# Optimization experiments

Hardware: AMD Instinct MI355X
Metric: run time of the kernel (lower is better)

Reference implementation:

```python
import jax, jax.numpy as jnp
import numpy as np

N, E, G = 40000, 400000, 64
IN, ED, HID, HEADS, OUT = 2, 18, 64, 4, 3

def _glorot(key, shape):
    fan_in = shape[0]
    return jax.random.normal(key, shape, dtype=jnp.float32) / np.float32(np.sqrt(fan_in))

def setup_inputs():
    key = jax.random.key(0)
    ks = jax.random.split(key, 32)
    d1 = HEADS * HID  # 256
    return {
        "x": jax.random.normal(ks[0], (N, IN), jnp.float32),
        "edge_index": jax.random.randint(ks[1], (2, E), 0, N),
        "edge_attr": jax.random.normal(ks[2], (E, ED), jnp.float32),
        "batch": jnp.sort(jax.random.randint(ks[3], (N,), 0, G)),
        # conv1: TransformerConv(2 -> 64, heads=4, concat=True, beta=True, edge_dim=18)
        "Wq1": _glorot(ks[4], (IN, d1)), "bq1": jnp.zeros((d1,), jnp.float32),
        "Wk1": _glorot(ks[5], (IN, d1)), "bk1": jnp.zeros((d1,), jnp.float32),
        "Wv1": _glorot(ks[6], (IN, d1)), "bv1": jnp.zeros((d1,), jnp.float32),
        "We1": _glorot(ks[7], (ED, d1)),
        "Wskip1": _glorot(ks[8], (IN, d1)), "bskip1": jnp.zeros((d1,), jnp.float32),
        "Wbeta1": _glorot(ks[9], (3 * d1, 1)),
        # conv2: TransformerConv(256 -> 64, heads=1, concat=False, beta=True, edge_dim=18)
        "Wq2": _glorot(ks[10], (d1, HID)), "bq2": jnp.zeros((HID,), jnp.float32),
        "Wk2": _glorot(ks[11], (d1, HID)), "bk2": jnp.zeros((HID,), jnp.float32),
        "Wv2": _glorot(ks[12], (d1, HID)), "bv2": jnp.zeros((HID,), jnp.float32),
        "We2": _glorot(ks[13], (ED, HID)),
        "Wskip2": _glorot(ks[14], (d1, HID)), "bskip2": jnp.zeros((HID,), jnp.float32),
        "Wbeta2": _glorot(ks[15], (3 * HID, 1)),
        "Wlin": _glorot(ks[16], (HID, OUT)), "blin": jnp.zeros((OUT,), jnp.float32),
    }

def _tconv(x, src, dst, edge_attr, Wq, bq, Wk, bk, Wv, bv, We, Wskip, bskip, Wbeta, H, C, concat):
    # PyG TransformerConv with edge_dim, beta=True, root_weight=True (eval: dropout off)
    n = x.shape[0]
    q = (x @ Wq + bq).reshape(n, H, C)
    k = (x @ Wk + bk).reshape(n, H, C)
    v = (x @ Wv + bv).reshape(n, H, C)
    e = (edge_attr @ We).reshape(-1, H, C)              # [E,H,C]
    kj = k[src] + e                                      # key_j + edge
    alpha = jnp.einsum('ehc,ehc->eh', q[dst], kj) * (1.0 / (C ** 0.5))  # [E,H]
    # segment softmax over destination nodes
    amax = jax.ops.segment_max(alpha, dst, num_segments=n)
    ex = jnp.exp(alpha - amax[dst])
    den = jax.ops.segment_sum(ex, dst, num_segments=n)
    w = ex / (den[dst] + 1e-16)
    msg = (v[src] + e) * w[:, :, None]                   # [E,H,C]
    out = jax.ops.segment_sum(msg, dst, num_segments=n)  # [N,H,C]
    out = out.reshape(n, H * C) if concat else out.mean(axis=1)
    # beta-gated skip connection
    xr = x @ Wskip + bskip
    beta = jax.nn.sigmoid(jnp.concatenate([out, xr, out - xr], axis=-1) @ Wbeta)
    return beta * xr + (1.0 - beta) * out

def reference(x, edge_index, edge_attr, batch, Wq1, bq1, Wk1, bk1, Wv1, bv1, We1, Wskip1, bskip1, Wbeta1, Wq2, bq2, Wk2, bk2, Wv2, bv2, We2, Wskip2, bskip2, Wbeta2, Wlin, blin):
    src, dst = edge_index[0], edge_index[1]
    h = jax.nn.relu(_tconv(x, src, dst, edge_attr, Wq1, bq1, Wk1, bk1, Wv1, bv1, We1, Wskip1, bskip1, Wbeta1, HEADS, HID, True))
    h = jax.nn.relu(_tconv(h, src, dst, edge_attr, Wq2, bq2, Wk2, bk2, Wv2, bv2, We2, Wskip2, bskip2, Wbeta2, 1, HID, False))
    # global mean pool per graph
    s = jax.ops.segment_sum(h, batch, num_segments=G)
    cnt = jax.ops.segment_sum(jnp.ones((h.shape[0], 1), h.dtype), batch, num_segments=G)
    pooled = s / jnp.maximum(cnt, 1.0)
    return pooled @ Wlin + blin
```

## Files before the change

### kernel.cpp

```cpp
#include <hip/hip_runtime.h>
#include <hip/hip_fp16.h>

#define N_NODES 40000
#define N_EDGES 400000
#define N_GRAPHS 64
#define D1 256
#define HIDC 64
#define NHEADS 4
#define EDIM 18
#define EPAD 20
#define OUTF 3

typedef _Float16 f16x8 __attribute__((ext_vector_type(8)));
typedef float f32x4 __attribute__((ext_vector_type(4)));

__global__ void prep_w(const float* __restrict__ Wq, const float* __restrict__ bq,
                       const float* __restrict__ Wk, const float* __restrict__ bk,
                       const float* __restrict__ Wv, const float* __restrict__ bv,
                       const float* __restrict__ Ws, const float* __restrict__ bs,
                       const float* __restrict__ We2,
                       const float* __restrict__ Wq1, const float* __restrict__ bq1,
                       const float* __restrict__ Wk1, const float* __restrict__ bk1,
                       const float* __restrict__ We1,
                       __half* __restrict__ Bt, float* __restrict__ bias,
                       float* __restrict__ cbuf) {
    int c = blockIdx.x, k = threadIdx.x;
    if (c < 256) {
        int m = c >> 6, d = c & 63;
        const float* W = (m == 0) ? Wq : (m == 1) ? Wk : (m == 2) ? Wv : Ws;
        Bt[c * 256 + k] = __float2half(W[k * 64 + d]);
        if (k == 0) {
            const float* b = (m == 0) ? bq : (m == 1) ? bk : (m == 2) ? bv : bs;
            bias[c] = b[d];
        }
    } else if (c < 288) {
        int j = c - 256;
        float s = 0.f;
        if (j < EDIM)
            for (int cc = 0; cc < 64; ++cc) s += Wq[k * 64 + cc] * We2[j * 64 + cc];
        Bt[c * 256 + k] = __float2half(s);
        if (k == 0) {
            float b = 0.f;
            if (j < EDIM)
                for (int cc = 0; cc < 64; ++cc) b += bq[cc] * We2[j * 64 + cc];
            bias[c] = b;
        }
    } else {
        int t = k;
        if (t < 36) {
            int h = t / 9, r = t % 9, a = r / 3, b = r % 3;
            const float* A = (a == 0) ? Wq1 : (a == 1) ? Wq1 + D1 : bq1;
            const float* B = (b == 0) ? Wk1 : (b == 1) ? Wk1 + D1 : bk1;
            float s = 0.f;
            for (int cc = 0; cc < 64; ++cc) s += A[h * 64 + cc] * B[h * 64 + cc];
            cbuf[h * 63 + a * 3 + b] = s;
        } else if (t < 252) {
            int i = t - 36;
            int h = i / 54, rr = (i % 54) / 18, j = i % 18;
            const float* A = (rr == 0) ? Wq1 : (rr == 1) ? Wq1 + D1 : bq1;
            float s = 0.f;
            for (int cc = 0; cc < 64; ++cc) s += A[h * 64 + cc] * We1[j * D1 + h * 64 + cc];
            cbuf[h * 63 + 9 + rr * 18 + j] = s;
        }
    }
}

__global__ void initA(const float* __restrict__ x, const float* __restrict__ cbuf,
                      float* __restrict__ coef, float* __restrict__ acc1,
                      float* __restrict__ acc2, float* __restrict__ out2,
                      int* __restrict__ deg, float* __restrict__ pooled,
                      int* __restrict__ gs, int* __restrict__ ge) {
    int t = blockIdx.x * 256 + threadIdx.x;
    acc1[t] = 0.f;
    {
        int n = t / 84, r = t % 84, h = r / 21, c = r % 21;
        const float* cb = cbuf + h * 63;
        float x0 = x[2 * n], x1 = x[2 * n + 1], o;
        if (c < 3) o = x0 * cb[c] + x1 * cb[3 + c] + cb[6 + c];
        else { int j = c - 3; o = x0 * cb[9 + j] + x1 * cb[27 + j] + cb[45 + j]; }
        coef[t] = o;
    }
    if (t < N_NODES * 64) out2[t] = 0.f;
    if (t < N_NODES * 20) acc2[t] = 0.f;
    if (t < N_NODES) deg[t] = 0;
    if (t < N_GRAPHS * HIDC) pooled[t] = 0.f;
    if (t < N_GRAPHS) { gs[t] = 0; ge[t] = 0; }
}

__global__ void hist_kernel(const int* __restrict__ ei, int* __restrict__ deg) {
    int e = blockIdx.x * 256 + threadIdx.x;
    if (e < N_EDGES) atomicAdd(&deg[ei[N_EDGES + e]], 1);
}

__global__ void scanA(const int* __restrict__ deg, int* __restrict__ bsum) {
    __shared__ int s[256];
    int b = blockIdx.x, t = threadIdx.x;
    s[t] = (t < 160) ? deg[b * 160 + t] : 0;
    __syncthreads();
    for (int off = 128; off; off >>= 1) {
        if (t < off) s[t] += s[t + off];
        __syncthreads();
    }
    if (t == 0) bsum[b] = s[0];
}

__global__ void scanB(const int* __restrict__ bsum, int* __restrict__ boff) {
    __shared__ int s[256];
    int t = threadIdx.x;
    int v = (t < 250) ? bsum[t] : 0;
    s[t] = v;
    __syncthreads();
    for (int off = 1; off < 256; off <<= 1) {
        int add = (t >= off) ? s[t - off] : 0;
        __syncthreads();
        s[t] += add;
        __syncthreads();
    }
    if (t < 250) boff[t] = s[t] - v;
}

__global__ void scanC(const int* __restrict__ deg, const int* __restrict__ boff,
                      int* __restrict__ cursor) {
    __shared__ int s[256];
    int b = blockIdx.x, t = threadIdx.x;
    int v = (t < 160) ? deg[b * 160 + t] : 0;
    s[t] = v;
    __syncthreads();
    for (int off = 1; off < 256; off <<= 1) {
        int add = (t >= off) ? s[t - off] : 0;
        __syncthreads();
        s[t] += add;
        __syncthreads();
    }
    if (t < 160) cursor[b * 160 + t] = boff[b] + s[t] - v;
}

__global__ void perm_kernel(const int* __restrict__ ei, int* __restrict__ cursor,
                            int* __restrict__ inv) {
    int e = blockIdx.x * 256 + threadIdx.x;
    if (e >= N_EDGES) return;
    int p = atomicAdd(&cursor[ei[N_EDGES + e]], 1);
    inv[p] = e;
}

__global__ void gatherE(const int* __restrict__ inv, const int* __restrict__ ei,
                        const float* __restrict__ ea, const float* __restrict__ x,
                        const float* __restrict__ coef,
                        int* __restrict__ src_s, int* __restrict__ dst_s,
                        float* __restrict__ ea_s, float* __restrict__ alpha1) {
    int p = blockIdx.x * 256 + threadIdx.x;
    if (p >= N_EDGES) return;
    int e = inv[p];
    int src = ei[e], dst = ei[N_EDGES + e];
    src_s[p] = src;
    dst_s[p] = dst;
    const float* srow = ea + (size_t)e * EDIM;
    float s[EDIM];
    #pragma unroll
    for (int j = 0; j < EDIM; ++j) s[j] = srow[j];
    float x0 = x[src * 2], x1 = x[src * 2 + 1];
    float4* drow = (float4*)(ea_s + (size_t)p * EPAD);
    drow[0] = make_float4(s[0],  s[1],  s[2],  s[3]);
    drow[1] = make_float4(s[4],  s[5],  s[6],  s[7]);
    drow[2] = make_float4(s[8],  s[9],  s[10], s[11]);
    drow[3] = make_float4(s[12], s[13], s[14], s[15]);
    drow[4] = make_float4(s[16], s[17], x0, x1);
    const float* cb = coef + (size_t)dst * 84;
    #pragma unroll
    for (int h = 0; h < NHEADS; ++h) {
        const float* c = cb + h * 21;
        float a = x0 * c[0] + x1 * c[1] + c[2];
        #pragma unroll
        for (int j = 0; j < EDIM; ++j) a += s[j] * c[3 + j];
        alpha1[(size_t)h * N_EDGES + p] = __expf(a * 0.125f);
    }
}

__global__ void strip1(const int* __restrict__ dst_s, const float* __restrict__ alpha1,
                       const float* __restrict__ ea_s, float* __restrict__ acc1) {
    int t = threadIdx.x;
    int strip = blockIdx.x * 2 + (t >> 7);
    int gl = t & 127;
    bool active = gl < 84;
    int cgl = active ? gl : 83;
    int h = cgl / 21, comp = cgl % 21;
    int voff = (comp == 0) ? 18 : (comp == 1) ? 19 : (comp - 3);
    bool isone = (comp == 2);
    int p0 = strip * 16;
    int dsts[16]; float w[16]; float v[16];
    #pragma unroll
    for (int j = 0; j < 16; ++j) dsts[j] = dst_s[p0 + j];
    #pragma unroll
    for (int j = 0; j < 16; ++j) w[j] = alpha1[(size_t)h * N_EDGES + p0 + j];
    #pragma unroll
    for (int j = 0; j < 16; ++j) v[j] = isone ? 1.f : ea_s[(size_t)(p0 + j) * EPAD + voff];
    float acc = 0.f;
    int prev = dsts[0];
    #pragma unroll
    for (int j = 0; j < 16; ++j) {
        if (dsts[j] != prev) {
            if (active) atomicAdd(&acc1[(size_t)prev * 84 + gl], acc);
            acc = 0.f; prev = dsts[j];
        }
        acc += w[j] * v[j];
    }
    if (active) atomicAdd(&acc1[(size_t)prev * 84 + gl], acc);
}

__global__ void finalize1x(const float* __restrict__ x, const float* __restrict__ acc1,
                           const float* __restrict__ Wv, const float* __restrict__ bv,
                           const float* __restrict__ We, const float* __restrict__ Wskip,
                           const float* __restrict__ bskip, const float* __restrict__ Wbeta,
                           __half* __restrict__ h1f) {
    __shared__ float red[4][4];
    int nb = blockIdx.x * 4;
    int t = threadIdx.x;
    int h = t >> 6;
    float wv0 = Wv[t], wv1 = Wv[D1 + t], bvv = bv[t];
    float we[EDIM];
    #pragma unroll
    for (int j = 0; j < EDIM; ++j) we[j] = We[j * D1 + t];
    float ws0 = Wskip[t], ws1 = Wskip[D1 + t], bsv = bskip[t];
    float wb0 = Wbeta[t], wb1 = Wbeta[D1 + t], wb2 = Wbeta[2 * D1 + t];
    float o[4], xr[4], part[4];
    #pragma unroll
    for (int i = 0; i < 4; ++i) {
        int node = nb + i;
        const float* a = acc1 + (size_t)node * 84 + h * 21;
        float l = a[2];
        float oo = a[0] * wv0 + a[1] * wv1 + l * bvv;
        #pragma unroll
        for (int j = 0; j < EDIM; ++j) oo += a[3 + j] * we[j];
        oo /= (l + 1e-16f);
        float x0 = x[node * 2], x1 = x[node * 2 + 1];
        xr[i] = x0 * ws0 + x1 * ws1 + bsv;
        o[i] = oo;
        part[i] = oo * wb0 + xr[i] * wb1 + (oo - xr[i]) * wb2;
    }
    #pragma unroll
    for (int off = 32; off; off >>= 1) {
        #pragma unroll
        for (int i = 0; i < 4; ++i) part[i] += __shfl_xor(part[i], off);
    }
    if ((t & 63) == 0) {
        #pragma unroll
        for (int i = 0; i < 4; ++i) red[h][i] = part[i];
    }
    __syncthreads();
    #pragma unroll
    for (int i = 0; i < 4; ++i) {
        float tot = red[0][i] + red[1][i] + red[2][i] + red[3][i];
        float beta = 1.f / (1.f + __expf(-tot));
        h1f[(size_t)(nb + i) * D1 + t] =
            __float2half(fmaxf(beta * xr[i] + (1.f - beta) * o[i], 0.f));
    }
}

__device__ __forceinline__ void nl2_store(int c, int gr, float v,
        float* __restrict__ q2, float* __restrict__ k2, __half* __restrict__ v2h,
        float* __restrict__ xr2, float* __restrict__ qe) {
    if (c < 256) {
        int m = c >> 6, d = c & 63;
        if (m == 0)      q2[(size_t)gr * 64 + d] = v;
        else if (m == 1) k2[(size_t)gr * 64 + d] = v;
        else if (m == 2) v2h[(size_t)gr * 64 + d] = __float2half(v);
        else             xr2[(size_t)gr * 64 + d] = v;
    } else {
        qe[(size_t)gr * 32 + (c - 256)] = v;
    }
}

__global__ __launch_bounds__(256) void nl2_mfma(
        const __half* __restrict__ h1f, const __half* __restrict__ Bt,
        const float* __restrict__ bias,
        float* __restrict__ q2, float* __restrict__ k2,
        __half* __restrict__ v2h, float* __restrict__ xr2,
        float* __restrict__ qe) {
    int W = blockIdx.x * 4 + (threadIdx.x >> 6);
    if (W >= 18 * 313) return;
    int ct = W % 18, chunk = W / 18;
    int lane = threadIdx.x & 63, quad = lane >> 4, mm = lane & 15;
    int c0 = ct * 16 + mm;
    const _Float16* Ap = (const _Float16*)h1f;
    const _Float16* Bp = (const _Float16*)Bt;
    const _Float16* b0 = Bp + (size_t)c0 * 256 + quad * 8;
    f16x8 b[8];
    #pragma unroll
    for (int s = 0; s < 8; ++s) b[s] = *(const f16x8*)(b0 + s * 32);
    float bz = bias[c0];
    int rt_end = chunk * 8 + 8; if (rt_end > 2500) rt_end = 2500;
    for (int rt = chunk * 8; rt < rt_end; ++rt) {
        int row0 = rt * 16;
        const _Float16* arow = Ap + (size_t)(row0 + mm) * 256 + quad * 8;
        f16x8 a[8];
        #pragma unroll
        for (int s = 0; s < 8; ++s) a[s] = *(const f16x8*)(arow + s * 32);
        f32x4 accA = {bz, bz, bz, bz};
        f32x4 accB = {0.f, 0.f, 0.f, 0.f};
        #pragma unroll
        for (int s = 0; s < 4; ++s) {
            accA = __builtin_amdgcn_mfma_f32_16x16x32_f16(a[s],     b[s],     accA, 0, 0, 0);
            accB = __builtin_amdgcn_mfma_f32_16x16x32_f16(a[s + 4], b[s + 4], accB, 0, 0, 0);
        }
        #pragma unroll
        for (int r = 0; r < 4; ++r) {
            int gr = row0 + quad * 4 + r;
            nl2_store(c0, gr, accA[r] + accB[r], q2, k2, v2h, xr2, qe);
        }
    }
}

#define LG2_BLOCKS 2048
#define LG2_WAVES (LG2_BLOCKS * 4)
__global__ void logits2(const int* __restrict__ src_s, const int* __restrict__ dst_s,
                        const float* __restrict__ ea_s, const float* __restrict__ q2,
                        const float* __restrict__ k2, const float* __restrict__ qe,
                        float* __restrict__ alpha2) {
    int t = threadIdx.x, wid = t >> 6, lane = t & 63;
    int w = blockIdx.x * 4 + wid;
    for (int base = w; base < N_EDGES; base += 2 * LG2_WAVES) {
        int p1 = base, p2 = base + LG2_WAVES;
        bool has2 = p2 < N_EDGES;
        int p2c = has2 ? p2 : p1;
        int s1 = src_s[p1], d1 = dst_s[p1];
        int s2 = src_s[p2c], d2 = dst_s[p2c];
        float dd1 = q2[(size_t)d1 * 64 + lane] * k2[(size_t)s1 * 64 + lane];
        float dd2 = q2[(size_t)d2 * 64 + lane] * k2[(size_t)s2 * 64 + lane];
        if (lane < 20) {
            dd1 += qe[(size_t)d1 * 32 + lane] * ea_s[(size_t)p1 * EPAD + lane];
            dd2 += qe[(size_t)d2 * 32 + lane] * ea_s[(size_t)p2c * EPAD + lane];
        }
        #pragma unroll
        for (int off = 32; off; off >>= 1) {
            dd1 += __shfl_xor(dd1, off);
            dd2 += __shfl_xor(dd2, off);
        }
        if (lane == 0) {
            alpha2[p1] = __expf(dd1 * 0.125f);
            if (has2) alpha2[p2] = __expf(dd2 * 0.125f);
        }
    }
}

__global__ void spmm2s(const int* __restrict__ dst_s, const int* __restrict__ src_s,
                       const float* __restrict__ alpha2, const __half* __restrict__ v2h,
                       const float* __restrict__ ea_s,
                       float* __restrict__ out2, float* __restrict__ acc2) {
    int t = threadIdx.x;
    int strip = blockIdx.x * 4 + (t >> 6);
    int lane = t & 63;
    int p0 = strip * 16;
    int dsts[16]; int srcs[16]; float w[16];
    #pragma unroll
    for (int j = 0; j < 16; ++j) dsts[j] = dst_s[p0 + j];
    #pragma unroll
    for (int j = 0; j < 16; ++j) srcs[j] = src_s[p0 + j];
    #pragma unroll
    for (int j = 0; j < 16; ++j) w[j] = alpha2[p0 + j];
    float vv[16]; float ev[16];
    #pragma unroll
    for (int j = 0; j < 16; ++j) vv[j] = __half2float(v2h[(size_t)srcs[j] * 64 + lane]);
    #pragma unroll
    for (int j = 0; j < 16; ++j)
        ev[j] = (lane < EDIM) ? ea_s[(size_t)(p0 + j) * EPAD + lane] : 1.f;
    float acc = 0.f, accS = 0.f;
    int prev = dsts[0];
    #pragma unroll
    for (int j = 0; j < 16; ++j) {
        if (dsts[j] != prev) {
            atomicAdd(&out2[(size_t)prev * 64 + lane], acc);
            if (lane < 19) atomicAdd(&acc2[(size_t)prev * 20 + lane], accS);
            acc = 0.f; accS = 0.f; prev = dsts[j];
        }
        acc += w[j] * vv[j];
        accS += w[j] * ev[j];
    }
    atomicAdd(&out2[(size_t)prev * 64 + lane], acc);
    if (lane < 19) atomicAdd(&acc2[(size_t)prev * 20 + lane], accS);
}

__global__ void finalize2x(const float* __restrict__ out2, const float* __restrict__ acc2,
                           const float* __restrict__ xr2, const float* __restrict__ We2,
                           const float* __restrict__ Wb2, float* __restrict__ h2) {
    __shared__ float w2s[EDIM * 64];
    int t = threadIdx.x;
    for (int i = t; i < EDIM * 64; i += 256) w2s[i] = We2[i];
    __syncthreads();
    int node = blockIdx.x * 4 + (t >> 6);
    int lane = t & 63;
    const float* a2 = acc2 + (size_t)node * 20;
    float num = out2[(size_t)node * 64 + lane];
    #pragma unroll
    for (int j = 0; j < EDIM; ++j) num += a2[j] * w2s[j * 64 + lane];
    float o = num / (a2[18] + 1e-16f);
    float xr = xr2[(size_t)node * 64 + lane];
    float part = o * Wb2[lane] + xr * Wb2[64 + lane] + (o - xr) * Wb2[128 + lane];
    #pragma unroll
    for (int off = 32; off; off >>= 1) part += __shfl_xor(part, off);
    float beta = 1.f / (1.f + __expf(-part));
    h2[(size_t)node * 64 + lane] = fmaxf(beta * xr + (1.f - beta) * o, 0.f);
}

__global__ void bounds_kernel(const int* __restrict__ batch, int* __restrict__ gs,
                              int* __restrict__ ge) {
    int n = blockIdx.x * 256 + threadIdx.x;
    if (n >= N_NODES) return;
    int b = batch[n];
    if (n == 0) gs[b] = 0;
    else { int pb = batch[n - 1]; if (pb != b) { ge[pb] = n; gs[b] = n; } }
    if (n == N_NODES - 1) ge[b] = N_NODES;
}

__global__ void pool_kernel(const float* __restrict__ h2, const int* __restrict__ gs,
                            const int* __restrict__ ge, float* __restrict__ pooled,
                            float* __restrict__ cnt) {
    __shared__ float red[4][64];
    int g = blockIdx.x >> 2, q = blockIdx.x & 3;
    int t = threadIdx.x, wv = t >> 6, lane = t & 63;
    int s = gs[g], e = ge[g];
    float sum = 0.f;
    for (int n = s + q * 4 + wv; n < e; n += 16) sum += h2[(size_t)n * 64 + lane];
    red[wv][lane] = sum;
    __syncthreads();
    if (wv == 0) {
        float v = red[0][lane] + red[1][lane] + red[2][lane] + red[3][lane];
        atomicAdd(&pooled[g * 64 + lane], v);
    }
    if (q == 0 && t == 0) cnt[g] = (float)(e - s);
}

__global__ void final_lin(const float* __restrict__ pooled, const float* __restrict__ cnt,
                          const float* __restrict__ Wlin, const float* __restrict__ blin,
                          float* __restrict__ out) {
    int t = threadIdx.x;
    if (t >= N_GRAPHS * OUTF) return;
    int g = t / OUTF, o = t % OUTF;
    float inv = 1.f / fmaxf(cnt[g], 1.f);
    float acc = 0.f;
    for (int kk = 0; kk < HIDC; ++kk) acc += pooled[g * 64 + kk] * Wlin[kk * OUTF + o];
    out[t] = acc * inv + blin[o];
}

extern "C" void kernel_launch(void* const* d_in, const int* in_sizes, int n_in,
                              void* d_out, int out_size, void* d_ws, size_t ws_size,
                              hipStream_t stream) {
    const float* x      = (const float*)d_in[0];
    const int*   ei     = (const int*)d_in[1];
    const float* ea     = (const float*)d_in[2];
    const int*   batch  = (const int*)d_in[3];
    const float* Wq1    = (const float*)d_in[4];  const float* bq1    = (const float*)d_in[5];
    const float* Wk1    = (const float*)d_in[6];  const float* bk1    = (const float*)d_in[7];
    const float* Wv1    = (const float*)d_in[8];  const float* bv1    = (const float*)d_in[9];
    const float* We1    = (const float*)d_in[10];
    const float* Wskip1 = (const float*)d_in[11]; const float* bskip1 = (const float*)d_in[12];
    const float* Wbeta1 = (const float*)d_in[13];
    const float* Wq2    = (const float*)d_in[14]; const float* bq2    = (const float*)d_in[15];
    const float* Wk2    = (const float*)d_in[16]; const float* bk2    = (const float*)d_in[17];
    const float* Wv2    = (const float*)d_in[18]; const float* bv2    = (const float*)d_in[19];
    const float* We2    = (const float*)d_in[20];
    const float* Wskip2 = (const float*)d_in[21]; const float* bskip2 = (const float*)d_in[22];
    const float* Wbeta2 = (const float*)d_in[23];
    const float* Wlin   = (const float*)d_in[24]; const float* blin   = (const float*)d_in[25];

    float* ptr = (float*)d_ws;
    float* q2     = ptr; ptr += (size_t)N_NODES * 64;
    float* k2     = ptr; ptr += (size_t)N_NODES * 64;
    float* xr2    = ptr; ptr += (size_t)N_NODES * 64;
    float* qe     = ptr; ptr += (size_t)N_NODES * 32;
    __half* v2h   = (__half*)ptr; ptr += (size_t)N_NODES * 32;
    float* ea_s   = ptr; ptr += (size_t)N_EDGES * EPAD;
    float* alpha2 = ptr; ptr += N_EDGES;
    float* acc2   = ptr; ptr += (size_t)N_NODES * 20;
    float* out2   = ptr; ptr += (size_t)N_NODES * 64;
    float* pooled = ptr; ptr += N_GRAPHS * HIDC;
    float* cnt    = ptr; ptr += N_GRAPHS;
    int*   gs     = (int*)ptr; ptr += N_GRAPHS;
    int*   ge     = (int*)ptr; ptr += N_GRAPHS;
    float* cbuf   = ptr; ptr += 256;
    float* bias   = ptr; ptr += 320;
    __half* Bt    = (__half*)ptr; ptr += (288 * 256) / 2;
    int*   src_s  = (int*)ptr; ptr += N_EDGES;
    int*   dst_s  = (int*)ptr; ptr += N_EDGES;
    int*   inv    = (int*)ptr; ptr += N_EDGES;
    int*   deg    = (int*)ptr; ptr += N_NODES;
    int*   cursor = (int*)ptr; ptr += N_NODES;
    int*   bsum   = (int*)ptr; ptr += 256;
    int*   boff   = (int*)ptr; ptr += 256;
    float* coef   = ptr; ptr += (size_t)N_NODES * 84;
    float* h2     = coef;
    float* acc1   = ptr; ptr += (size_t)N_NODES * 84;
    float* alpha1 = ptr; ptr += (size_t)4 * N_EDGES;
    __half* h1f   = (__half*)ptr; ptr += (size_t)N_NODES * 128;

    const int EB = (N_EDGES + 255) / 256;
    const int NB = (N_NODES + 255) / 256;

    prep_w<<<289, 256, 0, stream>>>(Wq2, bq2, Wk2, bk2, Wv2, bv2, Wskip2, bskip2, We2,
                                    Wq1, bq1, Wk1, bk1, We1, Bt, bias, cbuf);
    initA<<<(N_NODES * 84) / 256, 256, 0, stream>>>(x, cbuf, coef, acc1, acc2, out2,
                                                    deg, pooled, gs, ge);
    hist_kernel<<<EB, 256, 0, stream>>>(ei, deg);
    scanA<<<250, 256, 0, stream>>>(deg, bsum);
    scanB<<<1, 256, 0, stream>>>(bsum, boff);
    scanC<<<250, 256, 0, stream>>>(deg, boff, cursor);
    perm_kernel<<<EB, 256, 0, stream>>>(ei, cursor, inv);
    gatherE<<<EB, 256, 0, stream>>>(inv, ei, ea, x, coef, src_s, dst_s, ea_s, alpha1);

    strip1<<<(N_EDGES / 16) / 2, 256, 0, stream>>>(dst_s, alpha1, ea_s, acc1);
    finalize1x<<<N_NODES / 4, 256, 0, stream>>>(x, acc1, Wv1, bv1, We1, Wskip1, bskip1,
                                                Wbeta1, h1f);

    nl2_mfma<<<1409, 256, 0, stream>>>(h1f, Bt, bias, q2, k2, v2h, xr2, qe);
    logits2<<<LG2_BLOCKS, 256, 0, stream>>>(src_s, dst_s, ea_s, q2, k2, qe, alpha2);
    spmm2s<<<(N_EDGES / 16) / 4, 256, 0, stream>>>(dst_s, src_s, alpha2, v2h, ea_s,
                                                   out2, acc2);
    finalize2x<<<N_NODES / 4, 256, 0, stream>>>(out2, acc2, xr2, We2, Wbeta2, h2);

    bounds_kernel<<<NB, 256, 0, stream>>>(batch, gs, ge);
    pool_kernel<<<N_GRAPHS * 4, 256, 0, stream>>>(h2, gs, ge, pooled, cnt);
    final_lin<<<1, 256, 0, stream>>>(pooled, cnt, Wlin, blin, (float*)d_out);
}
```

Measured before the change: 449.8 us.

## Stage node-layer-2 input rows in LDS and fold graph-bounds into histogram

The layer-2 projection GEMM now loads a 64-row tile of h1 into padded shared memory once per block, and four waves reuse it across all 18 column tiles. Before, each wave re-read its A rows from global memory for every column tile. Separately, the graph-boundary computation is folded into the histogram kernel and the per-graph count buffer is dropped, with final_lin deriving counts from gs/ge. Together these remove one launch and redundant A traffic, at the cost of reloading B fragments per column tile and using more LDS per block.

```diff
diff --git a/kernel.cpp b/kernel.cpp
--- a/kernel.cpp
+++ b/kernel.cpp
@@ -10,6 +10,7 @@
 #define EDIM 18
 #define EPAD 20
 #define OUTF 3
+#define APAD 264
 
 typedef _Float16 f16x8 __attribute__((ext_vector_type(8)));
 typedef float f32x4 __attribute__((ext_vector_type(4)));
@@ -87,9 +88,18 @@
     if (t < N_GRAPHS) { gs[t] = 0; ge[t] = 0; }
 }
 
-__global__ void hist_kernel(const int* __restrict__ ei, int* __restrict__ deg) {
+__global__ void hist_kernel(const int* __restrict__ ei, int* __restrict__ deg,
+                            const int* __restrict__ batch, int* __restrict__ gs,
+                            int* __restrict__ ge) {
     int e = blockIdx.x * 256 + threadIdx.x;
     if (e < N_EDGES) atomicAdd(&deg[ei[N_EDGES + e]], 1);
+    int n = e;
+    if (n < N_NODES) {
+        int b = batch[n];
+        if (n == 0) gs[b] = 0;
+        else { int pb = batch[n - 1]; if (pb != b) { ge[pb] = n; gs[b] = n; } }
+        if (n == N_NODES - 1) ge[b] = N_NODES;
+    }
 }
 
 __global__ void scanA(const int* __restrict__ deg, int* __restrict__ bsum) {
@@ -276,36 +286,44 @@
         float* __restrict__ q2, float* __restrict__ k2,
         __half* __restrict__ v2h, float* __restrict__ xr2,
         float* __restrict__ qe) {
-    int W = blockIdx.x * 4 + (threadIdx.x >> 6);
-    if (W >= 18 * 313) return;
-    int ct = W % 18, chunk = W / 18;
-    int lane = threadIdx.x & 63, quad = lane >> 4, mm = lane & 15;
-    int c0 = ct * 16 + mm;
-    const _Float16* Ap = (const _Float16*)h1f;
+    __shared__ _Float16 As[64 * APAD];
+    int t = threadIdx.x;
+    int row0 = blockIdx.x * 64;
+    const float4* gsrc = (const float4*)(h1f + (size_t)row0 * 256);
+    #pragma unroll
+    for (int i = 0; i < 8; ++i) {
+        int li = i * 256 + t;
+        int r = li >> 5, c8 = li & 31;
+        *(float4*)(As + r * APAD + c8 * 8) = gsrc[li];
+    }
+    __syncthreads();
+    int wave = t >> 6, lane = t & 63, quad = lane >> 4, mm = lane & 15;
     const _Float16* Bp = (const _Float16*)Bt;
-    const _Float16* b0 = Bp + (size_t)c0 * 256 + quad * 8;
-    f16x8 b[8];
-    #pragma unroll
-    for (int s = 0; s < 8; ++s) b[s] = *(const f16x8*)(b0 + s * 32);
-    float bz = bias[c0];
-    int rt_end = chunk * 8 + 8; if (rt_end > 2500) rt_end = 2500;
-    for (int rt = chunk * 8; rt < rt_end; ++rt) {
-        int row0 = rt * 16;
-        const _Float16* arow = Ap + (size_t)(row0 + mm) * 256 + quad * 8;
-        f16x8 a[8];
-        #pragma unroll
-        for (int s = 0; s < 8; ++s) a[s] = *(const f16x8*)(arow + s * 32);
-        f32x4 accA = {bz, bz, bz, bz};
-        f32x4 accB = {0.f, 0.f, 0.f, 0.f};
-        #pragma unroll
-        for (int s = 0; s < 4; ++s) {
-            accA = __builtin_amdgcn_mfma_f32_16x16x32_f16(a[s],     b[s],     accA, 0, 0, 0);
-            accB = __builtin_amdgcn_mfma_f32_16x16x32_f16(a[s + 4], b[s + 4], accB, 0, 0, 0);
-        }
-        #pragma unroll
-        for (int r = 0; r < 4; ++r) {
-            int gr = row0 + quad * 4 + r;
-            nl2_store(c0, gr, accA[r] + accB[r], q2, k2, v2h, xr2, qe);
+    for (int ct = wave; ct < 18; ct += 4) {
+        int c0 = ct * 16 + mm;
+        const _Float16* b0 = Bp + (size_t)c0 * 256 + quad * 8;
+        f16x8 b[8];
+        #pragma unroll
+        for (int s = 0; s < 8; ++s) b[s] = *(const f16x8*)(b0 + s * 32);
+        float bz = bias[c0];
+        #pragma unroll
+        for (int rt = 0; rt < 4; ++rt) {
+            const _Float16* arow = As + (rt * 16 + mm) * APAD + quad * 8;
+            f16x8 a[8];
+            #pragma unroll
+            for (int s = 0; s < 8; ++s) a[s] = *(const f16x8*)(arow + s * 32);
+            f32x4 accA = {bz, bz, bz, bz};
+            f32x4 accB = {0.f, 0.f, 0.f, 0.f};
+            #pragma unroll
+            for (int s = 0; s < 4; ++s) {
+                accA = __builtin_amdgcn_mfma_f32_16x16x32_f16(a[s],     b[s],     accA, 0, 0, 0);
+                accB = __builtin_amdgcn_mfma_f32_16x16x32_f16(a[s + 4], b[s + 4], accB, 0, 0, 0);
+            }
+            #pragma unroll
+            for (int r = 0; r < 4; ++r) {
+                int gr = row0 + rt * 16 + quad * 4 + r;
+                nl2_store(c0, gr, accA[r] + accB[r], q2, k2, v2h, xr2, qe);
+            }
         }
     }
 }
@@ -401,19 +419,8 @@
     h2[(size_t)node * 64 + lane] = fmaxf(beta * xr + (1.f - beta) * o, 0.f);
 }
 
-__global__ void bounds_kernel(const int* __restrict__ batch, int* __restrict__ gs,
-                              int* __restrict__ ge) {
-    int n = blockIdx.x * 256 + threadIdx.x;
-    if (n >= N_NODES) return;
-    int b = batch[n];
-    if (n == 0) gs[b] = 0;
-    else { int pb = batch[n - 1]; if (pb != b) { ge[pb] = n; gs[b] = n; } }
-    if (n == N_NODES - 1) ge[b] = N_NODES;
-}
-
 __global__ void pool_kernel(const float* __restrict__ h2, const int* __restrict__ gs,
-                            const int* __restrict__ ge, float* __restrict__ pooled,
-                            float* __restrict__ cnt) {
+                            const int* __restrict__ ge, float* __restrict__ pooled) {
     __shared__ float red[4][64];
     int g = blockIdx.x >> 2, q = blockIdx.x & 3;
     int t = threadIdx.x, wv = t >> 6, lane = t & 63;
@@ -426,16 +433,17 @@
         float v = red[0][lane] + red[1][lane] + red[2][lane] + red[3][lane];
         atomicAdd(&pooled[g * 64 + lane], v);
     }
-    if (q == 0 && t == 0) cnt[g] = (float)(e - s);
-}
-
-__global__ void final_lin(const float* __restrict__ pooled, const float* __restrict__ cnt,
+}
+
+__global__ void final_lin(const float* __restrict__ pooled, const int* __restrict__ gs,
+                          const int* __restrict__ ge,
                           const float* __restrict__ Wlin, const float* __restrict__ blin,
                           float* __restrict__ out) {
     int t = threadIdx.x;
     if (t >= N_GRAPHS * OUTF) return;
     int g = t / OUTF, o = t % OUTF;
-    float inv = 1.f / fmaxf(cnt[g], 1.f);
+    int c = ge[g] - gs[g];
+    float inv = 1.f / fmaxf((float)c, 1.f);
     float acc = 0.f;
     for (int kk = 0; kk < HIDC; ++kk) acc += pooled[g * 64 + kk] * Wlin[kk * OUTF + o];
     out[t] = acc * inv + blin[o];
@@ -473,7 +481,6 @@
     float* acc2   = ptr; ptr += (size_t)N_NODES * 20;
     float* out2   = ptr; ptr += (size_t)N_NODES * 64;
     float* pooled = ptr; ptr += N_GRAPHS * HIDC;
-    float* cnt    = ptr; ptr += N_GRAPHS;
     int*   gs     = (int*)ptr; ptr += N_GRAPHS;
     int*   ge     = (int*)ptr; ptr += N_GRAPHS;
     float* cbuf   = ptr; ptr += 256;
@@ -493,13 +500,12 @@
     __half* h1f   = (__half*)ptr; ptr += (size_t)N_NODES * 128;
 
     const int EB = (N_EDGES + 255) / 256;
-    const int NB = (N_NODES + 255) / 256;
 
     prep_w<<<289, 256, 0, stream>>>(Wq2, bq2, Wk2, bk2, Wv2, bv2, Wskip2, bskip2, We2,
                                     Wq1, bq1, Wk1, bk1, We1, Bt, bias, cbuf);
     initA<<<(N_NODES * 84) / 256, 256, 0, stream>>>(x, cbuf, coef, acc1, acc2, out2,
                                                     deg, pooled, gs, ge);
-    hist_kernel<<<EB, 256, 0, stream>>>(ei, deg);
+    hist_kernel<<<EB, 256, 0, stream>>>(ei, deg, batch, gs, ge);
     scanA<<<250, 256, 0, stream>>>(deg, bsum);
     scanB<<<1, 256, 0, stream>>>(bsum, boff);
     scanC<<<250, 256, 0, stream>>>(deg, boff, cursor);
@@ -510,13 +516,12 @@
     finalize1x<<<N_NODES / 4, 256, 0, stream>>>(x, acc1, Wv1, bv1, We1, Wskip1, bskip1,
                                                 Wbeta1, h1f);
 
-    nl2_mfma<<<1409, 256, 0, stream>>>(h1f, Bt, bias, q2, k2, v2h, xr2, qe);
+    nl2_mfma<<<N_NODES / 64, 256, 0, stream>>>(h1f, Bt, bias, q2, k2, v2h, xr2, qe);
     logits2<<<LG2_BLOCKS, 256, 0, stream>>>(src_s, dst_s, ea_s, q2, k2, qe, alpha2);
     spmm2s<<<(N_EDGES / 16) / 4, 256, 0, stream>>>(dst_s, src_s, alpha2, v2h, ea_s,
                                                    out2, acc2);
     finalize2x<<<N_NODES / 4, 256, 0, stream>>>(out2, acc2, xr2, We2, Wbeta2, h2);
 
-    bounds_kernel<<<NB, 256, 0, stream>>>(batch, gs, ge);
-    pool_kernel<<<N_GRAPHS * 4, 256, 0, stream>>>(h2, gs, ge, pooled, cnt);
-    final_lin<<<1, 256, 0, stream>>>(pooled, cnt, Wlin, blin, (float*)d_out);
-}
+    pool_kernel<<<N_GRAPHS * 4, 256, 0, stream>>>(h2, gs, ge, pooled);
+    final_lin<<<1, 256, 0, stream>>>(pooled, gs, ge, Wlin, blin, (float*)d_out);
+}
```

New measurement: 436.8 us. 2.9% less time.
